# Optimization experiments

Measured on AMD Instinct MI355X. Metric: run time of the kernel, lower is better.

Reference implementation:

```python
import jax, jax.numpy as jnp
import numpy as np

B, S, T = 256, 64, 20
VIN, VOUT, E, H = 32000, 32000, 100, 1024
START_IDX = 1


def gru_cell(gi, h, W_hh, b_hh):
    # gi: precomputed input-side gates [B,3H] (order r,z,n as in PyTorch)
    gh = h @ W_hh.T + b_hh
    ir, iz, inn = jnp.split(gi, 3, axis=-1)
    hr, hz, hn = jnp.split(gh, 3, axis=-1)
    r = jax.nn.sigmoid(ir + hr)
    z = jax.nn.sigmoid(iz + hz)
    n = jnp.tanh(inn + r * hn)
    return (1.0 - z) * n + z * h


def setup_inputs() -> dict:
    key = jax.random.key(0)
    ks = jax.random.split(key, 16)
    sc = 0.05
    inputs = jax.random.randint(ks[0], (B, S), 0, VIN)
    targets = jax.random.randint(ks[1], (B, T), 0, VOUT)
    lengths = jax.random.randint(ks[2], (B,), 1, S + 1)
    h0_enc = jax.random.normal(ks[3], (1, B, H))
    E_enc = jax.random.normal(ks[4], (VIN, E)) * sc
    E_dec = jax.random.normal(ks[5], (VOUT, E)) * sc
    W_ih_e = jax.random.normal(ks[6], (3 * H, E)) * sc
    W_hh_e = jax.random.normal(ks[7], (3 * H, H)) * sc
    b_ih_e = jax.random.normal(ks[8], (3 * H,)) * sc
    b_hh_e = jax.random.normal(ks[9], (3 * H,)) * sc
    W_ih_d = jax.random.normal(ks[10], (3 * H, E + H)) * sc
    W_hh_d = jax.random.normal(ks[11], (3 * H, H)) * sc
    b_ih_d = jax.random.normal(ks[12], (3 * H,)) * sc
    b_hh_d = jax.random.normal(ks[13], (3 * H,)) * sc
    W_fc = jax.random.normal(ks[14], (VOUT, H)) * sc
    b_fc = jax.random.normal(ks[15], (VOUT,)) * sc
    return dict(inputs=inputs, targets=targets, lengths=lengths, h0_enc=h0_enc,
                E_enc=E_enc, E_dec=E_dec,
                W_ih_e=W_ih_e, W_hh_e=W_hh_e, b_ih_e=b_ih_e, b_hh_e=b_hh_e,
                W_ih_d=W_ih_d, W_hh_d=W_hh_d, b_ih_d=b_ih_d, b_hh_d=b_hh_d,
                W_fc=W_fc, b_fc=b_fc)


def reference(inputs, targets, lengths, h0_enc, E_enc, E_dec,
              W_ih_e, W_hh_e, b_ih_e, b_hh_e,
              W_ih_d, W_hh_d, b_ih_d, b_hh_d, W_fc, b_fc):
    Bsz, Slen = inputs.shape
    Tlen = targets.shape[1]
    # ---- Encoder GRU over padded inputs ----
    emb = E_enc[inputs]                       # [B,S,E]
    gi_all = emb @ W_ih_e.T + b_ih_e          # [B,S,3H] input-side gates, precomputed

    def enc_step(h, gi):
        h2 = gru_cell(gi, h, W_hh_e, b_hh_e)
        return h2, h2

    _, hs = jax.lax.scan(enc_step, h0_enc[0], jnp.swapaxes(gi_all, 0, 1))  # hs: [S,B,H]
    # pack_padded_sequence semantics: final hidden = hidden at step lengths-1
    context = hs[lengths - 1, jnp.arange(Bsz)]  # [B,H]

    # ---- Decoder: teacher-forced tokens are [start, targets[:,1:T-1]] ----
    dec_tokens = jnp.concatenate(
        [jnp.full((Bsz, 1), START_IDX, dtype=targets.dtype), targets[:, 1:Tlen - 1]], axis=1)  # [B,T-1]
    demb = E_dec[dec_tokens]                  # [B,T-1,E]
    ctx_b = jnp.broadcast_to(context[:, None, :], (Bsz, Tlen - 1, context.shape[-1]))
    x = jnp.concatenate([demb, ctx_b], axis=-1)          # [B,T-1,E+H]
    gi_d = x @ W_ih_d.T + b_ih_d                          # [B,T-1,3H]
    real = targets[:, 1:].T                               # [T-1,B]

    def dec_step(carry, inp):
        h, loss = carry
        gi, y = inp
        h2 = gru_cell(gi, h, W_hh_d, b_hh_d)
        logits = h2 @ W_fc.T + b_fc                       # [B,V]
        logp = jax.nn.log_softmax(logits, axis=-1)
        ce = -jnp.take_along_axis(logp, y[:, None], axis=1)[:, 0]  # [B]
        mask = (y >= 1).astype(logits.dtype)
        # faithful to: mean(CrossEntropyLoss(reduction='mean') * mask)
        step_loss = jnp.mean(ce) * jnp.mean(mask)
        return (h2, loss + step_loss), None

    init = (context, jnp.asarray(0.0, context.dtype))
    (_, loss), _ = jax.lax.scan(dec_step, init, (jnp.swapaxes(gi_d, 0, 1), real))
    return loss / Tlen
```

## Files before the change

### kernel.cpp

```cpp
#include <hip/hip_runtime.h>
#include <stdint.h>

#define BB 256
#define SS 64
#define TT 20
#define HH 1024
#define EE 100
#define G3 3072
#define G4 4096
#define KE 1152
#define VV 32000

typedef unsigned short ushort_t;
typedef unsigned long long u64_t;
typedef short bf16x8 __attribute__((ext_vector_type(8)));
typedef float f32x4 __attribute__((ext_vector_type(4)));

#define DEV static __device__ __forceinline__

DEV float bf2f(ushort_t h) {
    union { uint32_t u; float f; } c; c.u = ((uint32_t)h) << 16; return c.f;
}
DEV ushort_t f2bf(float x) {
    union { float f; uint32_t u; } c; c.f = x;
    uint32_t r = (c.u + 0x7fffu + ((c.u >> 16) & 1u)) >> 16;
    return (ushort_t)r;
}
DEV float sigm(float x) { return 1.f / (1.f + expf(-x)); }

DEV void storeC(float* p, float v) { *p = v; }
DEV void storeC(ushort_t* p, float v) { *p = f2bf(v); }

DEV u64_t ald(const void* p) {
    return __hip_atomic_load((const u64_t*)p, __ATOMIC_RELAXED, __HIP_MEMORY_SCOPE_AGENT);
}
DEV void ast(void* p, u64_t v) {
    __hip_atomic_store((u64_t*)p, v, __ATOMIC_RELAXED, __HIP_MEMORY_SCOPE_AGENT);
}

#define MFMA16(a, b, c) __builtin_amdgcn_mfma_f32_16x16x32_bf16(a, b, c, 0, 0, 0)

#define LGKM_BARRIER()                                         \
    do {                                                       \
        asm volatile("s_waitcnt lgkmcnt(0)" ::: "memory");     \
        __builtin_amdgcn_s_barrier();                          \
    } while (0)

DEV void groupbar(int* ctr, int target) {
    __syncthreads();
    if (threadIdx.x == 0) {
        __hip_atomic_fetch_add(ctr, 1, __ATOMIC_RELAXED, __HIP_MEMORY_SCOPE_AGENT);
        while (__hip_atomic_load(ctr, __ATOMIC_RELAXED, __HIP_MEMORY_SCOPE_AGENT) < target)
            __builtin_amdgcn_s_sleep(2);
    }
    __syncthreads();
    asm volatile("" ::: "memory");
}

__global__ void prep_w(const float* __restrict__ W_hh_e, const float* __restrict__ W_ih_e,
                       const float* __restrict__ W_ih_d,
                       ushort_t* __restrict__ W_enc_big, ushort_t* __restrict__ W_dec_pad) {
    int idx = blockIdx.x * 256 + threadIdx.x;
    int n = idx / 144, kc = (idx - n * 144) * 8;
    ushort_t o[8];
    if (n < G4) {
        if (kc < HH) {
            if (n < G3) {
#pragma unroll
                for (int u = 0; u < 8; ++u) o[u] = f2bf(W_hh_e[(size_t)n * HH + kc + u]);
            } else {
#pragma unroll
                for (int u = 0; u < 8; ++u) o[u] = 0;
            }
        } else {
            int kk = kc - HH;
#pragma unroll
            for (int u = 0; u < 8; ++u) {
                int k2 = kk + u;
                ushort_t v = 0;
                if (k2 < EE) {
                    if (n < 2048) v = f2bf(W_ih_e[(size_t)n * EE + k2]);
                    else if (n >= G3) v = f2bf(W_ih_e[(size_t)(n - HH) * EE + k2]);
                }
                o[u] = v;
            }
        }
        *(int4*)(W_enc_big + (size_t)n * KE + kc) = *(int4*)o;
    } else {
        int nd = n - G4;
        if (kc < 128) {
#pragma unroll
            for (int u = 0; u < 8; ++u) {
                int k2 = kc + u;
                o[u] = (k2 < EE) ? f2bf(W_ih_d[(size_t)nd * 1124 + k2]) : (ushort_t)0;
            }
        } else {
#pragma unroll
            for (int u = 0; u < 8; ++u) o[u] = f2bf(W_ih_d[(size_t)nd * 1124 + EE + (kc - 128) + u]);
        }
        *(int4*)(W_dec_pad + (size_t)nd * KE + kc) = *(int4*)o;
    }
}

__global__ void conv_w(const float* __restrict__ W_hh_d, const float* __restrict__ W_fc,
                       ushort_t* __restrict__ W_hhd_b, ushort_t* __restrict__ W_fc_b) {
    int idx = blockIdx.x * 256 + threadIdx.x;
    const int N1 = G3 * HH / 8;
    const float* src;
    ushort_t* dst;
    size_t e;
    if (idx < N1) { e = (size_t)idx * 8; src = W_hh_d; dst = W_hhd_b; }
    else { e = (size_t)(idx - N1) * 8; src = W_fc; dst = W_fc_b; }
    float4 a = *(const float4*)(src + e);
    float4 b = *(const float4*)(src + e + 4);
    ushort_t o[8] = {f2bf(a.x), f2bf(a.y), f2bf(a.z), f2bf(a.w),
                     f2bf(b.x), f2bf(b.y), f2bf(b.z), f2bf(b.w)};
    *(int4*)(dst + e) = *(int4*)o;
}

__global__ void prep_x(const int* __restrict__ inputs, const int* __restrict__ targets,
                       const float* __restrict__ h0, const float* __restrict__ E_enc,
                       const float* __restrict__ E_dec,
                       ushort_t* __restrict__ emb_pad, ushort_t* __restrict__ A_enc,
                       ushort_t* __restrict__ A_dec,
                       float* __restrict__ ce_sum, int* __restrict__ bar) {
    int idx = blockIdx.x * 256 + threadIdx.x;
    const int R0 = SS * BB * 128;
    const int R1 = R0 + BB * KE;
    const int R2 = R1 + (TT - 1) * BB * 128;
    const int R3 = R2 + 32 + 1024;
    if (idx < R0) {
        int s = idx >> 15;
        int r = idx & 32767;
        int b = r >> 7, k = r & 127;
        emb_pad[idx] = (k < EE) ? f2bf(E_enc[(size_t)inputs[b * SS + s] * EE + k]) : (ushort_t)0;
    } else if (idx < R1) {
        int i = idx - R0;
        int b = i / KE, c = i - b * KE;
        ushort_t v;
        if (c < HH) v = f2bf(h0[b * HH + c]);
        else { int kk = c - HH; v = (kk < EE) ? f2bf(E_enc[(size_t)inputs[b * SS] * EE + kk]) : (ushort_t)0; }
        A_enc[i] = v;
    } else if (idx < R2) {
        int i = idx - R1;
        int t = i >> 15;
        int r = i & 32767;
        int b = r >> 7, k = r & 127;
        int tok = (t == 0) ? 1 : targets[b * TT + t];
        A_dec[((size_t)(t * BB + b)) * KE + k] = (k < EE) ? f2bf(E_dec[(size_t)tok * EE + k]) : (ushort_t)0;
    } else if (idx < R2 + 32) {
        ce_sum[idx - R2] = 0.f;
    } else if (idx < R3) {
        bar[idx - R2 - 32] = 0;
    }
}

__global__ __launch_bounds__(256) void enc_all(
    ushort_t* __restrict__ A0, ushort_t* __restrict__ A1,
    const ushort_t* __restrict__ W, const float* __restrict__ bi,
    const float* __restrict__ bh, const float* __restrict__ h0,
    const ushort_t* __restrict__ emb_pad, const int* __restrict__ lengths,
    float* __restrict__ ctx_f, ushort_t* __restrict__ ctx_b, int* __restrict__ bar) {
    __shared__ __align__(16) ushort_t As[2][32 * 64];
    __shared__ float gbuf[4][32 * 33];
    int tid = threadIdx.x;
    int bid = blockIdx.x;
    int lane = tid & 63, g = tid >> 6;
    int jb = (bid & 7) * 4 + ((bid >> 3) & 3);
    int mg = bid >> 5;
    int j0 = jb << 5, m0 = mg << 5;
    int* barp = bar + mg * 64;
    int r16 = lane & 15, q = lane >> 4, q8 = q << 3;
    int srow = tid >> 3, skc = (tid & 7) << 3;
    const size_t offA = (size_t)(m0 + srow) * KE + skc;
    const int sx = (srow & 7) << 3;
    const int sw = (srow << 6) + (skc ^ sx);
    const ushort_t* wb0 = W + (size_t)(g * 1024 + j0 + r16) * KE + q8;
    const ushort_t* wb1 = wb0 + (size_t)16 * KE;
    int m = tid & 31, jc0 = (tid >> 5) << 2;
    int bgl = m0 + m, gjj = j0 + jc0;
    int len1 = lengths[bgl] - 1;
    float bir[4], bhr[4], biz[4], bhz[4], bhn[4], bin[4];
#pragma unroll
    for (int u = 0; u < 4; ++u) {
        int jg = gjj + u;
        bir[u] = bi[jg];        bhr[u] = bh[jg];
        biz[u] = bi[1024 + jg]; bhz[u] = bh[1024 + jg];
        bhn[u] = bh[2048 + jg]; bin[u] = bi[2048 + jg];
    }
    float hreg[4];
#pragma unroll
    for (int u = 0; u < 4; ++u) hreg[u] = h0[(size_t)bgl * HH + gjj + u];

#pragma unroll 1
    for (int s = 0; s < SS; ++s) {
        const ushort_t* Ain = (s & 1) ? A1 : A0;
        ushort_t* Aout = (s & 1) ? A0 : A1;
        const ushort_t* ap = Ain + offA;
        f32x4 zero = {0.f, 0.f, 0.f, 0.f};
        f32x4 acc[2][2];
        acc[0][0] = zero; acc[0][1] = zero; acc[1][0] = zero; acc[1][1] = zero;
        u64_t t0a = ald(ap), t0b = ald(ap + 4);
        u64_t b0a = ald(ap + 64), b0b = ald(ap + 68);
        u64_t b1a = ald(ap + 128), b1b = ald(ap + 132);
        bf16x8 wf00 = *(const bf16x8*)(wb0);
        bf16x8 wf01 = *(const bf16x8*)(wb1);
        bf16x8 wf10 = *(const bf16x8*)(wb0 + 32);
        bf16x8 wf11 = *(const bf16x8*)(wb1 + 32);
        { union { u64_t u[2]; int4 v; } st; st.u[0] = t0a; st.u[1] = t0b;
          *(int4*)(As[0] + sw) = st.v; }
        __syncthreads();
        const int NC = KE / 64;
#pragma unroll
        for (int c = 0; c < NC; ++c) {
            int kn = (c + 1) << 6;
            bf16x8 wn00, wn01, wn10, wn11;
            if (c + 1 < NC) {
                union { u64_t u[2]; int4 v; } st;
                if (c & 1) { st.u[0] = b1a; st.u[1] = b1b; }
                else       { st.u[0] = b0a; st.u[1] = b0b; }
                *(int4*)(As[(c + 1) & 1] + sw) = st.v;
                if (c + 3 < NC) {
                    int kf = (c + 3) << 6;
                    if (c & 1) { b1a = ald(ap + kf); b1b = ald(ap + kf + 4); }
                    else       { b0a = ald(ap + kf); b0b = ald(ap + kf + 4); }
                }
                wn00 = *(const bf16x8*)(wb0 + kn);
                wn01 = *(const bf16x8*)(wb1 + kn);
                wn10 = *(const bf16x8*)(wb0 + kn + 32);
                wn11 = *(const bf16x8*)(wb1 + kn + 32);
            }
            const ushort_t* Ab = As[c & 1];
#pragma unroll
            for (int i = 0; i < 2; ++i) {
                int row = (i << 4) + r16;
                int xr = (row & 7) << 3;
                bf16x8 af0 = *(const bf16x8*)(Ab + (row << 6) + (q8 ^ xr));
                bf16x8 af1 = *(const bf16x8*)(Ab + (row << 6) + ((q8 + 32) ^ xr));
                acc[i][0] = MFMA16(af0, wf00, acc[i][0]);
                acc[i][1] = MFMA16(af0, wf01, acc[i][1]);
                acc[i][0] = MFMA16(af1, wf10, acc[i][0]);
                acc[i][1] = MFMA16(af1, wf11, acc[i][1]);
            }
            if (c + 1 < NC) { wf00 = wn00; wf01 = wn01; wf10 = wn10; wf11 = wn11; }
            LGKM_BARRIER();
        }
#pragma unroll
        for (int i = 0; i < 2; ++i)
#pragma unroll
            for (int j2 = 0; j2 < 2; ++j2)
#pragma unroll
                for (int r = 0; r < 4; ++r)
                    gbuf[g][(i * 16 + q * 4 + r) * 33 + j2 * 16 + r16] = acc[i][j2][r];
        __syncthreads();
        int sel = (len1 == s);
        const float* gp0 = &gbuf[0][m * 33 + jc0];
        const float* gp1 = &gbuf[1][m * 33 + jc0];
        const float* gp2 = &gbuf[2][m * 33 + jc0];
        const float* gp3 = &gbuf[3][m * 33 + jc0];
        union { ushort_t s4[4]; u64_t u; } hb;
#pragma unroll
        for (int u = 0; u < 4; ++u) {
            float rr = sigm(gp0[u] + bir[u] + bhr[u]);
            float zz = sigm(gp1[u] + biz[u] + bhz[u]);
            float hn = gp2[u] + bhn[u];
            float inn = gp3[u] + bin[u];
            float nn = tanhf(inn + rr * hn);
            float h2 = (1.f - zz) * nn + zz * hreg[u];
            hreg[u] = h2;
            hb.s4[u] = f2bf(h2);
        }
        ast(Aout + (size_t)bgl * KE + gjj, hb.u);
        if (sel) {
            size_t hi = (size_t)bgl * 1024 + gjj;
            union { float f[2]; u64_t u; } c0, c1;
            c0.f[0] = hreg[0]; c0.f[1] = hreg[1];
            c1.f[0] = hreg[2]; c1.f[1] = hreg[3];
            ast(ctx_f + hi, c0.u); ast(ctx_f + hi + 2, c1.u);
            ast(ctx_b + hi, hb.u);
        }
        if (jb == 0 && s + 1 < SS) {
            int rr2 = tid >> 3, c0e = (tid & 7) << 4;
            const ushort_t* esrc = emb_pad + ((size_t)(s + 1) * BB + m0 + rr2) * 128 + c0e;
            union { int4 v; u64_t u[2]; } e0, e1;
            e0.v = *(const int4*)esrc;
            e1.v = *(const int4*)(esrc + 8);
            ushort_t* dst = Aout + (size_t)(m0 + rr2) * KE + 1024 + c0e;
            ast(dst, e0.u[0]); ast(dst + 4, e0.u[1]);
            ast(dst + 8, e1.u[0]); ast(dst + 12, e1.u[1]);
        }
        if (s + 1 < SS) groupbar(barp, (s + 1) * 32);
    }
}

__global__ void fill_ctx(const ushort_t* __restrict__ ctx_b, ushort_t* __restrict__ A_dec) {
    int idx = blockIdx.x * 256 + threadIdx.x;
    int t = idx >> 18;
    int r = idx & 262143;
    int b = r >> 10;
    int k = r & 1023;
    A_dec[((size_t)(t * BB + b)) * KE + 128 + k] = ctx_b[r];
}

template <typename OutT>
__global__ __launch_bounds__(256) void gemm128(const ushort_t* __restrict__ A,
                                               const ushort_t* __restrict__ W,
                                               OutT* __restrict__ C,
                                               int K, int lda, int ldw, int ldc) {
    __shared__ ushort_t As[2][128 * 32];
    __shared__ ushort_t Bs[2][128 * 32];
    int tid = threadIdx.x;
    int lane = tid & 63, wave = tid >> 6;
    int m0 = blockIdx.y << 7, n0 = blockIdx.x << 7;
    int row0 = tid >> 2, kc0 = (tid & 3) << 3;
    const ushort_t* a0p = A + (size_t)(m0 + row0) * lda + kc0;
    const ushort_t* a1p = A + (size_t)(m0 + row0 + 64) * lda + kc0;
    const ushort_t* w0p = W + (size_t)(n0 + row0) * ldw + kc0;
    const ushort_t* w1p = W + (size_t)(n0 + row0 + 64) * ldw + kc0;
    int mq = (wave >> 1) << 6, nq = (wave & 1) << 6;
    int r16 = lane & 15, q8 = (lane >> 4) << 3;
    const int sx = ((row0 >> 1) & 3) << 3;
    const int sw0 = (row0 << 5) + (kc0 ^ sx);
    const int sw1 = ((row0 + 64) << 5) + (kc0 ^ sx);
    f32x4 zero4 = {0.f, 0.f, 0.f, 0.f};
    f32x4 acc[4][4];
#pragma unroll
    for (int i = 0; i < 4; ++i)
#pragma unroll
        for (int j = 0; j < 4; ++j) acc[i][j] = zero4;
    int4 va0 = *(const int4*)(a0p);
    int4 va1 = *(const int4*)(a1p);
    int4 vb0 = *(const int4*)(w0p);
    int4 vb1 = *(const int4*)(w1p);
    *(int4*)(As[0] + sw0) = va0;
    *(int4*)(As[0] + sw1) = va1;
    *(int4*)(Bs[0] + sw0) = vb0;
    *(int4*)(Bs[0] + sw1) = vb1;
    va0 = *(const int4*)(a0p + 32);
    va1 = *(const int4*)(a1p + 32);
    vb0 = *(const int4*)(w0p + 32);
    vb1 = *(const int4*)(w1p + 32);
    __syncthreads();
    int p = 0;
    for (int k0 = 0; k0 < K; k0 += 32) {
        int kn = k0 + 32;
        if (kn < K) {
            *(int4*)(As[p ^ 1] + sw0) = va0;
            *(int4*)(As[p ^ 1] + sw1) = va1;
            *(int4*)(Bs[p ^ 1] + sw0) = vb0;
            *(int4*)(Bs[p ^ 1] + sw1) = vb1;
            if (kn + 32 < K) {
                va0 = *(const int4*)(a0p + kn + 32);
                va1 = *(const int4*)(a1p + kn + 32);
                vb0 = *(const int4*)(w0p + kn + 32);
                vb1 = *(const int4*)(w1p + kn + 32);
            }
        }
        bf16x8 af[4], bfv[4];
#pragma unroll
        for (int i = 0; i < 4; ++i) {
            int ar = mq + i * 16 + r16;
            af[i] = *(const bf16x8*)(As[p] + (ar << 5) + (q8 ^ ((((ar) >> 1) & 3) << 3)));
        }
#pragma unroll
        for (int j = 0; j < 4; ++j) {
            int br = nq + j * 16 + r16;
            bfv[j] = *(const bf16x8*)(Bs[p] + (br << 5) + (q8 ^ ((((br) >> 1) & 3) << 3)));
        }
#pragma unroll
        for (int i = 0; i < 4; ++i)
#pragma unroll
            for (int j = 0; j < 4; ++j) acc[i][j] = MFMA16(af[i], bfv[j], acc[i][j]);
        LGKM_BARRIER();
        p ^= 1;
    }
    int rbase = (lane >> 4) << 2;
#pragma unroll
    for (int i = 0; i < 4; ++i)
#pragma unroll
        for (int j = 0; j < 4; ++j)
#pragma unroll
            for (int r = 0; r < 4; ++r)
                storeC(&C[(size_t)(m0 + mq + i * 16 + rbase + r) * ldc + (n0 + nq + j * 16 + r16)],
                       acc[i][j][r]);
}

__global__ __launch_bounds__(256) void dec_all(
    const ushort_t* __restrict__ ctx_b, ushort_t* __restrict__ H_all,
    const ushort_t* __restrict__ W, const ushort_t* __restrict__ gi_all,
    const float* __restrict__ bi, const float* __restrict__ bh,
    const float* __restrict__ ctx_f, int* __restrict__ bar) {
    __shared__ __align__(16) ushort_t As[2][32 * 64];
    __shared__ float gbuf[3][32 * 33];
    int tid = threadIdx.x;
    int bid = blockIdx.x;
    int lane = tid & 63, g = tid >> 6;
    int jb = (bid & 7) * 4 + ((bid >> 3) & 3);
    int mg = bid >> 5;
    int j0 = jb << 5, m0 = mg << 5;
    int* barp = bar + 512 + mg * 64;
    int r16 = lane & 15, q = lane >> 4, q8 = q << 3;
    int srow = tid >> 3, skc = (tid & 7) << 3;
    const size_t offA = (size_t)(m0 + srow) * HH + skc;
    const int sx = (srow & 7) << 3;
    const int sw = (srow << 6) + (skc ^ sx);
    const ushort_t* wb0 = W + (size_t)(g * 1024 + j0 + r16) * HH + q8;
    const ushort_t* wb1 = wb0 + (size_t)16 * HH;
    int m = tid & 31, jc0 = (tid >> 5) << 2;
    int bgl = m0 + m, gjj = j0 + jc0;
    float bir[4], bhr[4], biz[4], bhz[4], bhn[4], bin[4];
#pragma unroll
    for (int u = 0; u < 4; ++u) {
        int jg = gjj + u;
        bir[u] = bi[jg];        bhr[u] = bh[jg];
        biz[u] = bi[1024 + jg]; bhz[u] = bh[1024 + jg];
        bhn[u] = bh[2048 + jg]; bin[u] = bi[2048 + jg];
    }
    float hreg[4];
#pragma unroll
    for (int u = 0; u < 4; ++u) hreg[u] = ctx_f[(size_t)bgl * HH + gjj + u];

#pragma unroll 1
    for (int t = 0; t < TT - 1; ++t) {
        const ushort_t* Ain = t ? (H_all + (size_t)(t - 1) * BB * HH) : ctx_b;
        ushort_t* Aout = H_all + (size_t)t * BB * HH;
        const ushort_t* ap = Ain + offA;
        f32x4 zero = {0.f, 0.f, 0.f, 0.f};
        f32x4 acc[2][2];
        acc[0][0] = zero; acc[0][1] = zero; acc[1][0] = zero; acc[1][1] = zero;
        u64_t t0a = ald(ap), t0b = ald(ap + 4);
        u64_t b0a = ald(ap + 64), b0b = ald(ap + 68);
        u64_t b1a = ald(ap + 128), b1b = ald(ap + 132);
        bf16x8 wf00 = {0, 0, 0, 0, 0, 0, 0, 0}, wf01 = wf00, wf10 = wf00, wf11 = wf00;
        if (g < 3) {
            wf00 = *(const bf16x8*)(wb0);
            wf01 = *(const bf16x8*)(wb1);
            wf10 = *(const bf16x8*)(wb0 + 32);
            wf11 = *(const bf16x8*)(wb1 + 32);
        }
        { union { u64_t u[2]; int4 v; } st; st.u[0] = t0a; st.u[1] = t0b;
          *(int4*)(As[0] + sw) = st.v; }
        __syncthreads();
        const int NC = HH / 64;
#pragma unroll
        for (int c = 0; c < NC; ++c) {
            int kn = (c + 1) << 6;
            bf16x8 wn00, wn01, wn10, wn11;
            if (c + 1 < NC) {
                union { u64_t u[2]; int4 v; } st;
                if (c & 1) { st.u[0] = b1a; st.u[1] = b1b; }
                else       { st.u[0] = b0a; st.u[1] = b0b; }
                *(int4*)(As[(c + 1) & 1] + sw) = st.v;
                if (c + 3 < NC) {
                    int kf = (c + 3) << 6;
                    if (c & 1) { b1a = ald(ap + kf); b1b = ald(ap + kf + 4); }
                    else       { b0a = ald(ap + kf); b0b = ald(ap + kf + 4); }
                }
                if (g < 3) {
                    wn00 = *(const bf16x8*)(wb0 + kn);
                    wn01 = *(const bf16x8*)(wb1 + kn);
                    wn10 = *(const bf16x8*)(wb0 + kn + 32);
                    wn11 = *(const bf16x8*)(wb1 + kn + 32);
                }
            }
            if (g < 3) {
                const ushort_t* Ab = As[c & 1];
#pragma unroll
                for (int i = 0; i < 2; ++i) {
                    int row = (i << 4) + r16;
                    int xr = (row & 7) << 3;
                    bf16x8 af0 = *(const bf16x8*)(Ab + (row << 6) + (q8 ^ xr));
                    bf16x8 af1 = *(const bf16x8*)(Ab + (row << 6) + ((q8 + 32) ^ xr));
                    acc[i][0] = MFMA16(af0, wf00, acc[i][0]);
                    acc[i][1] = MFMA16(af0, wf01, acc[i][1]);
                    acc[i][0] = MFMA16(af1, wf10, acc[i][0]);
                    acc[i][1] = MFMA16(af1, wf11, acc[i][1]);
                }
                if (c + 1 < NC) { wf00 = wn00; wf01 = wn01; wf10 = wn10; wf11 = wn11; }
            }
            LGKM_BARRIER();
        }
        if (g < 3) {
#pragma unroll
            for (int i = 0; i < 2; ++i)
#pragma unroll
                for (int j2 = 0; j2 < 2; ++j2)
#pragma unroll
                    for (int r = 0; r < 4; ++r)
                        gbuf[g][(i * 16 + q * 4 + r) * 33 + j2 * 16 + r16] = acc[i][j2][r];
        }
        __syncthreads();
        const ushort_t* gib = gi_all + ((size_t)t * BB + bgl) * G3;
        union { u64_t u; ushort_t s4[4]; } gr, gz, gn;
        gr.u = *(const u64_t*)(gib + gjj);
        gz.u = *(const u64_t*)(gib + 1024 + gjj);
        gn.u = *(const u64_t*)(gib + 2048 + gjj);
        const float* gp0 = &gbuf[0][m * 33 + jc0];
        const float* gp1 = &gbuf[1][m * 33 + jc0];
        const float* gp2 = &gbuf[2][m * 33 + jc0];
        union { ushort_t s4[4]; u64_t u; } hb;
#pragma unroll
        for (int u = 0; u < 4; ++u) {
            float rr = sigm(gp0[u] + bhr[u] + bf2f(gr.s4[u]) + bir[u]);
            float zz = sigm(gp1[u] + bhz[u] + bf2f(gz.s4[u]) + biz[u]);
            float hn = gp2[u] + bhn[u];
            float inn = bf2f(gn.s4[u]) + bin[u];
            float nn = tanhf(inn + rr * hn);
            float h2 = (1.f - zz) * nn + zz * hreg[u];
            hreg[u] = h2;
            hb.s4[u] = f2bf(h2);
        }
        ast(Aout + (size_t)bgl * 1024 + gjj, hb.u);
        if (t + 1 < TT - 1) groupbar(barp, (t + 1) * 32);
    }
}

__global__ __launch_bounds__(256) void logits_ce(
    const ushort_t* __restrict__ A, const ushort_t* __restrict__ Wf,
    const float* __restrict__ bfc, const int* __restrict__ targets,
    float* __restrict__ part_max, float* __restrict__ part_sum,
    float* __restrict__ xt) {
    int bid = blockIdx.x;
    int xcd = bid & 7;
    int slot = bid >> 3;
    int n_t = slot / 5;
    int m_t = xcd * 5 + (slot - n_t * 5);
    if (m_t >= (TT - 1) * BB / 128) return;
    __shared__ ushort_t As[2][128 * 32];
    __shared__ ushort_t Bs[2][128 * 32];
    __shared__ float wm[128][2], ws2[128][2];
    int tid = threadIdx.x;
    int lane = tid & 63, wave = tid >> 6;
    int m0 = m_t << 7, n0 = n_t << 7;
    int row0 = tid >> 2, kc0 = (tid & 3) << 3;
    const ushort_t* a0p = A + (size_t)(m0 + row0) * HH + kc0;
    const ushort_t* a1p = A + (size_t)(m0 + row0 + 64) * HH + kc0;
    const ushort_t* w0p = Wf + (size_t)(n0 + row0) * HH + kc0;
    const ushort_t* w1p = Wf + (size_t)(n0 + row0 + 64) * HH + kc0;
    int mq = (wave >> 1) << 6, nq = (wave & 1) << 6;
    int r16 = lane & 15, q = lane >> 4, q8 = q << 3;
    const int sx = ((row0 >> 1) & 3) << 3;
    const int sw0 = (row0 << 5) + (kc0 ^ sx);
    const int sw1 = ((row0 + 64) << 5) + (kc0 ^ sx);
    f32x4 zero4 = {0.f, 0.f, 0.f, 0.f};
    f32x4 acc[4][4];
#pragma unroll
    for (int i = 0; i < 4; ++i)
#pragma unroll
        for (int j = 0; j < 4; ++j) acc[i][j] = zero4;
    int4 va0 = *(const int4*)(a0p);
    int4 va1 = *(const int4*)(a1p);
    int4 vb0 = *(const int4*)(w0p);
    int4 vb1 = *(const int4*)(w1p);
    *(int4*)(As[0] + sw0) = va0;
    *(int4*)(As[0] + sw1) = va1;
    *(int4*)(Bs[0] + sw0) = vb0;
    *(int4*)(Bs[0] + sw1) = vb1;
    va0 = *(const int4*)(a0p + 32);
    va1 = *(const int4*)(a1p + 32);
    vb0 = *(const int4*)(w0p + 32);
    vb1 = *(const int4*)(w1p + 32);
    __syncthreads();
    int p = 0;
    for (int k0 = 0; k0 < HH; k0 += 32) {
        int kn = k0 + 32;
        if (kn < HH) {
            *(int4*)(As[p ^ 1] + sw0) = va0;
            *(int4*)(As[p ^ 1] + sw1) = va1;
            *(int4*)(Bs[p ^ 1] + sw0) = vb0;
            *(int4*)(Bs[p ^ 1] + sw1) = vb1;
            if (kn + 32 < HH) {
                va0 = *(const int4*)(a0p + kn + 32);
                va1 = *(const int4*)(a1p + kn + 32);
                vb0 = *(const int4*)(w0p + kn + 32);
                vb1 = *(const int4*)(w1p + kn + 32);
            }
        }
        bf16x8 af[4], bfv[4];
#pragma unroll
        for (int i = 0; i < 4; ++i) {
            int ar = mq + i * 16 + r16;
            af[i] = *(const bf16x8*)(As[p] + (ar << 5) + (q8 ^ ((((ar) >> 1) & 3) << 3)));
        }
#pragma unroll
        for (int j = 0; j < 4; ++j) {
            int br = nq + j * 16 + r16;
            bfv[j] = *(const bf16x8*)(Bs[p] + (br << 5) + (q8 ^ ((((br) >> 1) & 3) << 3)));
        }
#pragma unroll
        for (int i = 0; i < 4; ++i)
#pragma unroll
            for (int j = 0; j < 4; ++j) acc[i][j] = MFMA16(af[i], bfv[j], acc[i][j]);
        LGKM_BARRIER();
        p ^= 1;
    }
    float bias[4];
#pragma unroll
    for (int j2 = 0; j2 < 4; ++j2) bias[j2] = bfc[n0 + nq + j2 * 16 + r16];
    int nw = wave & 1;
#pragma unroll
    for (int i = 0; i < 4; ++i) {
#pragma unroll
        for (int r = 0; r < 4; ++r) {
            int rloc = mq + i * 16 + q * 4 + r;
            int brow = m0 + rloc;
            int y = targets[(brow & 255) * TT + (brow >> 8) + 1];
            float v[4];
            float mx = -3.0e38f;
#pragma unroll
            for (int j2 = 0; j2 < 4; ++j2) {
                v[j2] = acc[i][j2][r] + bias[j2];
                if (n0 + nq + j2 * 16 + r16 == y) xt[brow] = v[j2];
                mx = fmaxf(mx, v[j2]);
            }
#pragma unroll
            for (int d = 1; d < 16; d <<= 1) mx = fmaxf(mx, __shfl_xor(mx, d, 64));
            float se = 0.f;
#pragma unroll
            for (int j2 = 0; j2 < 4; ++j2) se += expf(v[j2] - mx);
#pragma unroll
            for (int d = 1; d < 16; d <<= 1) se += __shfl_xor(se, d, 64);
            if (r16 == 0) { wm[rloc][nw] = mx; ws2[rloc][nw] = se; }
        }
    }
    __syncthreads();
    if (tid < 128) {
        float m0v = wm[tid][0], m1v = wm[tid][1];
        float M = fmaxf(m0v, m1v);
        float S = ws2[tid][0] * expf(m0v - M) + ws2[tid][1] * expf(m1v - M);
        int brow = m0 + tid;
        part_max[(size_t)brow * 256 + n_t] = M;
        part_sum[(size_t)brow * 256 + n_t] = S;
    }
}

__global__ void ce_merge(const float* __restrict__ pm, const float* __restrict__ ps,
                         const float* __restrict__ xt, float* __restrict__ ce_sum) {
    int row = blockIdx.x * 4 + (threadIdx.x >> 6);
    int lane = threadIdx.x & 63;
    const float* pmr = pm + (size_t)row * 256;
    const float* psr = ps + (size_t)row * 256;
    float lm[4];
    int cnt = 0;
    float mx = -3.0e38f;
    for (int i = lane; i < 250; i += 64) { float v = pmr[i]; lm[cnt++] = v; mx = fmaxf(mx, v); }
    for (int d = 1; d < 64; d <<= 1) mx = fmaxf(mx, __shfl_xor(mx, d, 64));
    float s = 0.f;
    cnt = 0;
    for (int i = lane; i < 250; i += 64) { s += psr[i] * expf(lm[cnt++] - mx); }
    for (int d = 1; d < 64; d <<= 1) s += __shfl_xor(s, d, 64);
    if (lane == 0) atomicAdd(&ce_sum[row >> 8], mx + logf(s) - xt[row]);
}

__global__ void finalize(const float* __restrict__ ce_sum, const int* __restrict__ targets,
                         float* __restrict__ out) {
    int lane = threadIdx.x;
    float term = 0.f;
    if (lane < TT - 1) {
        int msum = 0;
        for (int b = 0; b < BB; ++b) msum += (targets[b * TT + lane + 1] >= 1) ? 1 : 0;
        term = (ce_sum[lane] * (1.f / BB)) * ((float)msum * (1.f / BB));
    }
    for (int off = 32; off > 0; off >>= 1) term += __shfl_down(term, off, 64);
    if (lane == 0) out[0] = term * (1.f / TT);
}

extern "C" void kernel_launch(void* const* d_in, const int* in_sizes, int n_in,
                              void* d_out, int out_size, void* d_ws, size_t ws_size,
                              hipStream_t stream) {
    const int* inputs = (const int*)d_in[0];
    const int* targets = (const int*)d_in[1];
    const int* lengths = (const int*)d_in[2];
    const float* h0 = (const float*)d_in[3];
    const float* E_enc = (const float*)d_in[4];
    const float* E_dec = (const float*)d_in[5];
    const float* W_ih_e = (const float*)d_in[6];
    const float* W_hh_e = (const float*)d_in[7];
    const float* b_ih_e = (const float*)d_in[8];
    const float* b_hh_e = (const float*)d_in[9];
    const float* W_ih_d = (const float*)d_in[10];
    const float* W_hh_d = (const float*)d_in[11];
    const float* b_ih_d = (const float*)d_in[12];
    const float* b_hh_d = (const float*)d_in[13];
    const float* W_fc = (const float*)d_in[14];
    const float* b_fc = (const float*)d_in[15];

    char* ws = (char*)d_ws;
    size_t off = 0;
    auto alloc = [&](size_t bytes) -> char* {
        char* p = ws + off;
        off += (bytes + 255) & ~(size_t)255;
        return p;
    };
    const int MROWS = (TT - 1) * BB;
    ushort_t* W_enc_big = (ushort_t*)alloc((size_t)G4 * KE * 2);
    ushort_t* W_dec_pad = (ushort_t*)alloc((size_t)G3 * KE * 2);
    ushort_t* W_hhd_b = (ushort_t*)alloc((size_t)G3 * HH * 2);
    ushort_t* W_fc_b = (ushort_t*)alloc((size_t)VV * HH * 2);
    ushort_t* emb_pad = (ushort_t*)alloc((size_t)SS * BB * 128 * 2);
    ushort_t* A_enc0 = (ushort_t*)alloc((size_t)BB * KE * 2);
    ushort_t* A_enc1 = (ushort_t*)alloc((size_t)BB * KE * 2);
    ushort_t* A_dec = (ushort_t*)alloc((size_t)MROWS * KE * 2);
    ushort_t* gi_dec = (ushort_t*)alloc((size_t)MROWS * G3 * 2);
    ushort_t* H_all = (ushort_t*)alloc((size_t)MROWS * HH * 2);
    float* ctx_f = (float*)alloc((size_t)BB * HH * 4);
    ushort_t* ctx_b = (ushort_t*)alloc((size_t)BB * HH * 2);
    float* part_max = (float*)alloc((size_t)MROWS * 256 * 4);
    float* part_sum = (float*)alloc((size_t)MROWS * 256 * 4);
    float* xt = (float*)alloc((size_t)MROWS * 4);
    float* ce_sum = (float*)alloc(64 * 4);
    int* bar = (int*)alloc(1024 * 4);

    prep_w<<<(G4 + G3) * (KE / 8) / 256, 256, 0, stream>>>(W_hh_e, W_ih_e, W_ih_d,
                                                           W_enc_big, W_dec_pad);
    conv_w<<<(G3 * HH + VV * HH) / 8 / 256, 256, 0, stream>>>(W_hh_d, W_fc, W_hhd_b, W_fc_b);
    {
        int nx = SS * BB * 128 + BB * KE + (TT - 1) * BB * 128 + 32 + 1024;
        prep_x<<<(nx + 255) / 256, 256, 0, stream>>>(inputs, targets, h0, E_enc, E_dec,
                                                     emb_pad, A_enc0, A_dec, ce_sum, bar);
    }

    enc_all<<<256, 256, 0, stream>>>(A_enc0, A_enc1, W_enc_big, b_ih_e, b_hh_e,
                                     h0, emb_pad, lengths, ctx_f, ctx_b, bar);

    fill_ctx<<<((TT - 1) * BB * HH) / 256, 256, 0, stream>>>(ctx_b, A_dec);
    gemm128<ushort_t><<<dim3(G3 / 128, MROWS / 128), 256, 0, stream>>>(
        A_dec, W_dec_pad, gi_dec, KE, KE, KE, G3);

    dec_all<<<256, 256, 0, stream>>>(ctx_b, H_all, W_hhd_b, gi_dec,
                                     b_ih_d, b_hh_d, ctx_f, bar);

    logits_ce<<<10000, 256, 0, stream>>>(H_all, W_fc_b, b_fc, targets,
                                         part_max, part_sum, xt);
    ce_merge<<<MROWS / 4, 256, 0, stream>>>(part_max, part_sum, xt, ce_sum);

    finalize<<<1, 64, 0, stream>>>(ce_sum, targets, (float*)d_out);
}
```

Baseline: 1.800 ms.

## Halve batch tile in persistent GRU kernels, launch 512 blocks, preload A rows

The persistent encoder and decoder recurrence kernels now give each block 16 batch rows instead of 32, so the grid doubles to 512 blocks at two blocks per CU. Each block loads all of its hidden-state chunks into registers at the start of a step instead of running a rolling three-stage prefetch. The barrier area is enlarged to hold the extra group counters. The intent is to spread the serial recurrence across more CUs and cut per-step latency. In exchange, every block re-reads the full weight slice, so weight traffic per step doubles, and the grid-wide spin barriers now have twice as many participants.

```diff
diff --git a/kernel.cpp b/kernel.cpp
--- a/kernel.cpp
+++ b/kernel.cpp
@@ -36,6 +36,9 @@
 }
 DEV void ast(void* p, u64_t v) {
     __hip_atomic_store((u64_t*)p, v, __ATOMIC_RELAXED, __HIP_MEMORY_SCOPE_AGENT);
+}
+DEV void ast32(void* p, uint32_t v) {
+    __hip_atomic_store((uint32_t*)p, v, __ATOMIC_RELAXED, __HIP_MEMORY_SCOPE_AGENT);
 }
 
 #define MFMA16(a, b, c) __builtin_amdgcn_mfma_f32_16x16x32_bf16(a, b, c, 0, 0, 0)
@@ -128,7 +131,7 @@
     const int R0 = SS * BB * 128;
     const int R1 = R0 + BB * KE;
     const int R2 = R1 + (TT - 1) * BB * 128;
-    const int R3 = R2 + 32 + 1024;
+    const int R3 = R2 + 32 + 2048;
     if (idx < R0) {
         int s = idx >> 15;
         int r = idx & 32767;
@@ -155,112 +158,95 @@
     }
 }
 
-__global__ __launch_bounds__(256) void enc_all(
+__global__ __launch_bounds__(256, 2) void enc_all(
     ushort_t* __restrict__ A0, ushort_t* __restrict__ A1,
     const ushort_t* __restrict__ W, const float* __restrict__ bi,
     const float* __restrict__ bh, const float* __restrict__ h0,
     const ushort_t* __restrict__ emb_pad, const int* __restrict__ lengths,
     float* __restrict__ ctx_f, ushort_t* __restrict__ ctx_b, int* __restrict__ bar) {
-    __shared__ __align__(16) ushort_t As[2][32 * 64];
-    __shared__ float gbuf[4][32 * 33];
+    __shared__ __align__(16) ushort_t As[2][16 * 64];
+    __shared__ float gbuf[4][16 * 33];
     int tid = threadIdx.x;
     int bid = blockIdx.x;
     int lane = tid & 63, g = tid >> 6;
     int jb = (bid & 7) * 4 + ((bid >> 3) & 3);
     int mg = bid >> 5;
-    int j0 = jb << 5, m0 = mg << 5;
+    int j0 = jb << 5, m0 = mg << 4;
     int* barp = bar + mg * 64;
     int r16 = lane & 15, q = lane >> 4, q8 = q << 3;
-    int srow = tid >> 3, skc = (tid & 7) << 3;
+    int srow = tid >> 4, skc = (tid & 15) << 2;
     const size_t offA = (size_t)(m0 + srow) * KE + skc;
-    const int sx = (srow & 7) << 3;
-    const int sw = (srow << 6) + (skc ^ sx);
+    const int sw = (srow << 6) + (skc ^ ((srow & 7) << 3));
     const ushort_t* wb0 = W + (size_t)(g * 1024 + j0 + r16) * KE + q8;
     const ushort_t* wb1 = wb0 + (size_t)16 * KE;
-    int m = tid & 31, jc0 = (tid >> 5) << 2;
+    int m = tid & 15, jc0 = (tid >> 4) << 1;
     int bgl = m0 + m, gjj = j0 + jc0;
     int len1 = lengths[bgl] - 1;
-    float bir[4], bhr[4], biz[4], bhz[4], bhn[4], bin[4];
-#pragma unroll
-    for (int u = 0; u < 4; ++u) {
+    float bir[2], bhr[2], biz[2], bhz[2], bhn[2], bin[2];
+#pragma unroll
+    for (int u = 0; u < 2; ++u) {
         int jg = gjj + u;
         bir[u] = bi[jg];        bhr[u] = bh[jg];
         biz[u] = bi[1024 + jg]; bhz[u] = bh[1024 + jg];
         bhn[u] = bh[2048 + jg]; bin[u] = bi[2048 + jg];
     }
-    float hreg[4];
-#pragma unroll
-    for (int u = 0; u < 4; ++u) hreg[u] = h0[(size_t)bgl * HH + gjj + u];
-
+    float hreg[2];
+#pragma unroll
+    for (int u = 0; u < 2; ++u) hreg[u] = h0[(size_t)bgl * HH + gjj + u];
+
+    const int NC = KE / 64;
 #pragma unroll 1
     for (int s = 0; s < SS; ++s) {
         const ushort_t* Ain = (s & 1) ? A1 : A0;
         ushort_t* Aout = (s & 1) ? A0 : A1;
         const ushort_t* ap = Ain + offA;
+        u64_t areg[NC];
+#pragma unroll
+        for (int c = 0; c < NC; ++c) areg[c] = ald(ap + (c << 6));
         f32x4 zero = {0.f, 0.f, 0.f, 0.f};
-        f32x4 acc[2][2];
-        acc[0][0] = zero; acc[0][1] = zero; acc[1][0] = zero; acc[1][1] = zero;
-        u64_t t0a = ald(ap), t0b = ald(ap + 4);
-        u64_t b0a = ald(ap + 64), b0b = ald(ap + 68);
-        u64_t b1a = ald(ap + 128), b1b = ald(ap + 132);
+        f32x4 acc0 = zero, acc1 = zero;
         bf16x8 wf00 = *(const bf16x8*)(wb0);
         bf16x8 wf01 = *(const bf16x8*)(wb1);
         bf16x8 wf10 = *(const bf16x8*)(wb0 + 32);
         bf16x8 wf11 = *(const bf16x8*)(wb1 + 32);
-        { union { u64_t u[2]; int4 v; } st; st.u[0] = t0a; st.u[1] = t0b;
-          *(int4*)(As[0] + sw) = st.v; }
-        __syncthreads();
-        const int NC = KE / 64;
+        *(u64_t*)(As[0] + sw) = areg[0];
+        LGKM_BARRIER();
 #pragma unroll
         for (int c = 0; c < NC; ++c) {
-            int kn = (c + 1) << 6;
             bf16x8 wn00, wn01, wn10, wn11;
             if (c + 1 < NC) {
-                union { u64_t u[2]; int4 v; } st;
-                if (c & 1) { st.u[0] = b1a; st.u[1] = b1b; }
-                else       { st.u[0] = b0a; st.u[1] = b0b; }
-                *(int4*)(As[(c + 1) & 1] + sw) = st.v;
-                if (c + 3 < NC) {
-                    int kf = (c + 3) << 6;
-                    if (c & 1) { b1a = ald(ap + kf); b1b = ald(ap + kf + 4); }
-                    else       { b0a = ald(ap + kf); b0b = ald(ap + kf + 4); }
-                }
+                *(u64_t*)(As[(c + 1) & 1] + sw) = areg[c + 1];
+                int kn = (c + 1) << 6;
                 wn00 = *(const bf16x8*)(wb0 + kn);
                 wn01 = *(const bf16x8*)(wb1 + kn);
                 wn10 = *(const bf16x8*)(wb0 + kn + 32);
                 wn11 = *(const bf16x8*)(wb1 + kn + 32);
             }
             const ushort_t* Ab = As[c & 1];
-#pragma unroll
-            for (int i = 0; i < 2; ++i) {
-                int row = (i << 4) + r16;
-                int xr = (row & 7) << 3;
-                bf16x8 af0 = *(const bf16x8*)(Ab + (row << 6) + (q8 ^ xr));
-                bf16x8 af1 = *(const bf16x8*)(Ab + (row << 6) + ((q8 + 32) ^ xr));
-                acc[i][0] = MFMA16(af0, wf00, acc[i][0]);
-                acc[i][1] = MFMA16(af0, wf01, acc[i][1]);
-                acc[i][0] = MFMA16(af1, wf10, acc[i][0]);
-                acc[i][1] = MFMA16(af1, wf11, acc[i][1]);
-            }
+            int xr = (r16 & 7) << 3;
+            bf16x8 af0 = *(const bf16x8*)(Ab + (r16 << 6) + (q8 ^ xr));
+            bf16x8 af1 = *(const bf16x8*)(Ab + (r16 << 6) + ((q8 + 32) ^ xr));
+            acc0 = MFMA16(af0, wf00, acc0);
+            acc1 = MFMA16(af0, wf01, acc1);
+            acc0 = MFMA16(af1, wf10, acc0);
+            acc1 = MFMA16(af1, wf11, acc1);
             if (c + 1 < NC) { wf00 = wn00; wf01 = wn01; wf10 = wn10; wf11 = wn11; }
             LGKM_BARRIER();
         }
 #pragma unroll
-        for (int i = 0; i < 2; ++i)
-#pragma unroll
-            for (int j2 = 0; j2 < 2; ++j2)
-#pragma unroll
-                for (int r = 0; r < 4; ++r)
-                    gbuf[g][(i * 16 + q * 4 + r) * 33 + j2 * 16 + r16] = acc[i][j2][r];
+        for (int r = 0; r < 4; ++r) {
+            gbuf[g][(q * 4 + r) * 33 + r16] = acc0[r];
+            gbuf[g][(q * 4 + r) * 33 + 16 + r16] = acc1[r];
+        }
         __syncthreads();
         int sel = (len1 == s);
         const float* gp0 = &gbuf[0][m * 33 + jc0];
         const float* gp1 = &gbuf[1][m * 33 + jc0];
         const float* gp2 = &gbuf[2][m * 33 + jc0];
         const float* gp3 = &gbuf[3][m * 33 + jc0];
-        union { ushort_t s4[4]; u64_t u; } hb;
-#pragma unroll
-        for (int u = 0; u < 4; ++u) {
+        union { ushort_t s2[2]; uint32_t u; } hb;
+#pragma unroll
+        for (int u = 0; u < 2; ++u) {
             float rr = sigm(gp0[u] + bir[u] + bhr[u]);
             float zz = sigm(gp1[u] + biz[u] + bhz[u]);
             float hn = gp2[u] + bhn[u];
@@ -268,26 +254,23 @@
             float nn = tanhf(inn + rr * hn);
             float h2 = (1.f - zz) * nn + zz * hreg[u];
             hreg[u] = h2;
-            hb.s4[u] = f2bf(h2);
-        }
-        ast(Aout + (size_t)bgl * KE + gjj, hb.u);
+            hb.s2[u] = f2bf(h2);
+        }
+        ast32(Aout + (size_t)bgl * KE + gjj, hb.u);
         if (sel) {
             size_t hi = (size_t)bgl * 1024 + gjj;
-            union { float f[2]; u64_t u; } c0, c1;
-            c0.f[0] = hreg[0]; c0.f[1] = hreg[1];
-            c1.f[0] = hreg[2]; c1.f[1] = hreg[3];
-            ast(ctx_f + hi, c0.u); ast(ctx_f + hi + 2, c1.u);
-            ast(ctx_b + hi, hb.u);
+            union { float f[2]; u64_t u; } cf;
+            cf.f[0] = hreg[0]; cf.f[1] = hreg[1];
+            ast(ctx_f + hi, cf.u);
+            ast32(ctx_b + hi, hb.u);
         }
         if (jb == 0 && s + 1 < SS) {
-            int rr2 = tid >> 3, c0e = (tid & 7) << 4;
+            int rr2 = tid >> 4, c0e = (tid & 15) << 3;
             const ushort_t* esrc = emb_pad + ((size_t)(s + 1) * BB + m0 + rr2) * 128 + c0e;
-            union { int4 v; u64_t u[2]; } e0, e1;
+            union { int4 v; u64_t u[2]; } e0;
             e0.v = *(const int4*)esrc;
-            e1.v = *(const int4*)(esrc + 8);
             ushort_t* dst = Aout + (size_t)(m0 + rr2) * KE + 1024 + c0e;
             ast(dst, e0.u[0]); ast(dst + 4, e0.u[1]);
-            ast(dst + 8, e1.u[0]); ast(dst + 12, e1.u[1]);
         }
         if (s + 1 < SS) groupbar(barp, (s + 1) * 32);
     }
@@ -385,52 +368,51 @@
                        acc[i][j][r]);
 }
 
-__global__ __launch_bounds__(256) void dec_all(
+__global__ __launch_bounds__(256, 2) void dec_all(
     const ushort_t* __restrict__ ctx_b, ushort_t* __restrict__ H_all,
     const ushort_t* __restrict__ W, const ushort_t* __restrict__ gi_all,
     const float* __restrict__ bi, const float* __restrict__ bh,
     const float* __restrict__ ctx_f, int* __restrict__ bar) {
-    __shared__ __align__(16) ushort_t As[2][32 * 64];
-    __shared__ float gbuf[3][32 * 33];
+    __shared__ __align__(16) ushort_t As[2][16 * 64];
+    __shared__ float gbuf[3][16 * 33];
     int tid = threadIdx.x;
     int bid = blockIdx.x;
     int lane = tid & 63, g = tid >> 6;
     int jb = (bid & 7) * 4 + ((bid >> 3) & 3);
     int mg = bid >> 5;
-    int j0 = jb << 5, m0 = mg << 5;
-    int* barp = bar + 512 + mg * 64;
+    int j0 = jb << 5, m0 = mg << 4;
+    int* barp = bar + 1024 + mg * 64;
     int r16 = lane & 15, q = lane >> 4, q8 = q << 3;
-    int srow = tid >> 3, skc = (tid & 7) << 3;
+    int srow = tid >> 4, skc = (tid & 15) << 2;
     const size_t offA = (size_t)(m0 + srow) * HH + skc;
-    const int sx = (srow & 7) << 3;
-    const int sw = (srow << 6) + (skc ^ sx);
+    const int sw = (srow << 6) + (skc ^ ((srow & 7) << 3));
     const ushort_t* wb0 = W + (size_t)(g * 1024 + j0 + r16) * HH + q8;
     const ushort_t* wb1 = wb0 + (size_t)16 * HH;
-    int m = tid & 31, jc0 = (tid >> 5) << 2;
+    int m = tid & 15, jc0 = (tid >> 4) << 1;
     int bgl = m0 + m, gjj = j0 + jc0;
-    float bir[4], bhr[4], biz[4], bhz[4], bhn[4], bin[4];
-#pragma unroll
-    for (int u = 0; u < 4; ++u) {
+    float bir[2], bhr[2], biz[2], bhz[2], bhn[2], bin[2];
+#pragma unroll
+    for (int u = 0; u < 2; ++u) {
         int jg = gjj + u;
         bir[u] = bi[jg];        bhr[u] = bh[jg];
         biz[u] = bi[1024 + jg]; bhz[u] = bh[1024 + jg];
         bhn[u] = bh[2048 + jg]; bin[u] = bi[2048 + jg];
     }
-    float hreg[4];
-#pragma unroll
-    for (int u = 0; u < 4; ++u) hreg[u] = ctx_f[(size_t)bgl * HH + gjj + u];
-
+    float hreg[2];
+#pragma unroll
+    for (int u = 0; u < 2; ++u) hreg[u] = ctx_f[(size_t)bgl * HH + gjj + u];
+
+    const int NC = HH / 64;
 #pragma unroll 1
     for (int t = 0; t < TT - 1; ++t) {
         const ushort_t* Ain = t ? (H_all + (size_t)(t - 1) * BB * HH) : ctx_b;
         ushort_t* Aout = H_all + (size_t)t * BB * HH;
         const ushort_t* ap = Ain + offA;
+        u64_t areg[NC];
+#pragma unroll
+        for (int c = 0; c < NC; ++c) areg[c] = ald(ap + (c << 6));
         f32x4 zero = {0.f, 0.f, 0.f, 0.f};
-        f32x4 acc[2][2];
-        acc[0][0] = zero; acc[0][1] = zero; acc[1][0] = zero; acc[1][1] = zero;
-        u64_t t0a = ald(ap), t0b = ald(ap + 4);
-        u64_t b0a = ald(ap + 64), b0b = ald(ap + 68);
-        u64_t b1a = ald(ap + 128), b1b = ald(ap + 132);
+        f32x4 acc0 = zero, acc1 = zero;
         bf16x8 wf00 = {0, 0, 0, 0, 0, 0, 0, 0}, wf01 = wf00, wf10 = wf00, wf11 = wf00;
         if (g < 3) {
             wf00 = *(const bf16x8*)(wb0);
@@ -438,25 +420,15 @@
             wf10 = *(const bf16x8*)(wb0 + 32);
             wf11 = *(const bf16x8*)(wb1 + 32);
         }
-        { union { u64_t u[2]; int4 v; } st; st.u[0] = t0a; st.u[1] = t0b;
-          *(int4*)(As[0] + sw) = st.v; }
-        __syncthreads();
-        const int NC = HH / 64;
+        *(u64_t*)(As[0] + sw) = areg[0];
+        LGKM_BARRIER();
 #pragma unroll
         for (int c = 0; c < NC; ++c) {
-            int kn = (c + 1) << 6;
             bf16x8 wn00, wn01, wn10, wn11;
             if (c + 1 < NC) {
-                union { u64_t u[2]; int4 v; } st;
-                if (c & 1) { st.u[0] = b1a; st.u[1] = b1b; }
-                else       { st.u[0] = b0a; st.u[1] = b0b; }
-                *(int4*)(As[(c + 1) & 1] + sw) = st.v;
-                if (c + 3 < NC) {
-                    int kf = (c + 3) << 6;
-                    if (c & 1) { b1a = ald(ap + kf); b1b = ald(ap + kf + 4); }
-                    else       { b0a = ald(ap + kf); b0b = ald(ap + kf + 4); }
-                }
+                *(u64_t*)(As[(c + 1) & 1] + sw) = areg[c + 1];
                 if (g < 3) {
+                    int kn = (c + 1) << 6;
                     wn00 = *(const bf16x8*)(wb0 + kn);
                     wn01 = *(const bf16x8*)(wb1 + kn);
                     wn10 = *(const bf16x8*)(wb0 + kn + 32);
@@ -465,52 +437,46 @@
             }
             if (g < 3) {
                 const ushort_t* Ab = As[c & 1];
-#pragma unroll
-                for (int i = 0; i < 2; ++i) {
-                    int row = (i << 4) + r16;
-                    int xr = (row & 7) << 3;
-                    bf16x8 af0 = *(const bf16x8*)(Ab + (row << 6) + (q8 ^ xr));
-                    bf16x8 af1 = *(const bf16x8*)(Ab + (row << 6) + ((q8 + 32) ^ xr));
-                    acc[i][0] = MFMA16(af0, wf00, acc[i][0]);
-                    acc[i][1] = MFMA16(af0, wf01, acc[i][1]);
-                    acc[i][0] = MFMA16(af1, wf10, acc[i][0]);
-                    acc[i][1] = MFMA16(af1, wf11, acc[i][1]);
-                }
+                int xr = (r16 & 7) << 3;
+                bf16x8 af0 = *(const bf16x8*)(Ab + (r16 << 6) + (q8 ^ xr));
+                bf16x8 af1 = *(const bf16x8*)(Ab + (r16 << 6) + ((q8 + 32) ^ xr));
+                acc0 = MFMA16(af0, wf00, acc0);
+                acc1 = MFMA16(af0, wf01, acc1);
+                acc0 = MFMA16(af1, wf10, acc0);
+                acc1 = MFMA16(af1, wf11, acc1);
                 if (c + 1 < NC) { wf00 = wn00; wf01 = wn01; wf10 = wn10; wf11 = wn11; }
             }
             LGKM_BARRIER();
         }
         if (g < 3) {
 #pragma unroll
-            for (int i = 0; i < 2; ++i)
-#pragma unroll
-                for (int j2 = 0; j2 < 2; ++j2)
-#pragma unroll
-                    for (int r = 0; r < 4; ++r)
-                        gbuf[g][(i * 16 + q * 4 + r) * 33 + j2 * 16 + r16] = acc[i][j2][r];
+            for (int r = 0; r < 4; ++r) {
+                gbuf[g][(q * 4 + r) * 33 + r16] = acc0[r];
+                gbuf[g][(q * 4 + r) * 33 + 16 + r16] = acc1[r];
+            }
         }
         __syncthreads();
         const ushort_t* gib = gi_all + ((size_t)t * BB + bgl) * G3;
-        union { u64_t u; ushort_t s4[4]; } gr, gz, gn;
-        gr.u = *(const u64_t*)(gib + gjj);
-        gz.u = *(const u64_t*)(gib + 1024 + gjj);
-        gn.u = *(const u64_t*)(gib + 2048 + gjj);
+        union { uint32_t u; ushort_t s2[2]; } gr, gz, gn;
+        gr.u = *(const uint32_t*)(gib + gjj);
+        gz.u = *(const uint32_t*)(gib + 1024 + gjj);
+        gn.u = *(const uint32_t*)(gib + 2048 + gjj);
         const float* gp0 = &gbuf[0][m * 33 + jc0];
         const float* gp1 = &gbuf[1][m * 33 + jc0];
         const float* gp2 = &gbuf[2][m * 33 + jc0];
-        union { ushort_t s4[4]; u64_t u; } hb;
-#pragma unroll
-        for (int u = 0; u < 4; ++u) {
-            float rr = sigm(gp0[u] + bhr[u] + bf2f(gr.s4[u]) + bir[u]);
-            float zz = sigm(gp1[u] + bhz[u] + bf2f(gz.s4[u]) + biz[u]);
+        union { ushort_t s2[2]; uint32_t u; } hb;
+#pragma unroll
+        for (int u = 0; u < 2; ++u) {
+            float rr = sigm(gp0[u] + bhr[u] + bf2f(gr.s2[u]) + bir[u]);
+            float zz = sigm(gp1[u] + bhz[u] + bf2f(gz.s2[u]) + biz[u]);
             float hn = gp2[u] + bhn[u];
-            float inn = bf2f(gn.s4[u]) + bin[u];
+            float inn = bf2f(gn.s2[u]) + bin[u];
             float nn = tanhf(inn + rr * hn);
             float h2 = (1.f - zz) * nn + zz * hreg[u];
             hreg[u] = h2;
-            hb.s4[u] = f2bf(h2);
-        }
-        ast(Aout + (size_t)bgl * 1024 + gjj, hb.u);
+            hb.s2[u] = f2bf(h2);
+        }
+        ast32(Aout + (size_t)bgl * 1024 + gjj, hb.u);
         if (t + 1 < TT - 1) groupbar(barp, (t + 1) * 32);
     }
 }
@@ -709,25 +675,25 @@
     float* part_sum = (float*)alloc((size_t)MROWS * 256 * 4);
     float* xt = (float*)alloc((size_t)MROWS * 4);
     float* ce_sum = (float*)alloc(64 * 4);
-    int* bar = (int*)alloc(1024 * 4);
+    int* bar = (int*)alloc(2048 * 4);
 
     prep_w<<<(G4 + G3) * (KE / 8) / 256, 256, 0, stream>>>(W_hh_e, W_ih_e, W_ih_d,
                                                            W_enc_big, W_dec_pad);
     conv_w<<<(G3 * HH + VV * HH) / 8 / 256, 256, 0, stream>>>(W_hh_d, W_fc, W_hhd_b, W_fc_b);
     {
-        int nx = SS * BB * 128 + BB * KE + (TT - 1) * BB * 128 + 32 + 1024;
+        int nx = SS * BB * 128 + BB * KE + (TT - 1) * BB * 128 + 32 + 2048;
         prep_x<<<(nx + 255) / 256, 256, 0, stream>>>(inputs, targets, h0, E_enc, E_dec,
                                                      emb_pad, A_enc0, A_dec, ce_sum, bar);
     }
 
-    enc_all<<<256, 256, 0, stream>>>(A_enc0, A_enc1, W_enc_big, b_ih_e, b_hh_e,
+    enc_all<<<512, 256, 0, stream>>>(A_enc0, A_enc1, W_enc_big, b_ih_e, b_hh_e,
                                      h0, emb_pad, lengths, ctx_f, ctx_b, bar);
 
     fill_ctx<<<((TT - 1) * BB * HH) / 256, 256, 0, stream>>>(ctx_b, A_dec);
     gemm128<ushort_t><<<dim3(G3 / 128, MROWS / 128), 256, 0, stream>>>(
         A_dec, W_dec_pad, gi_dec, KE, KE, KE, G3);
 
-    dec_all<<<256, 256, 0, stream>>>(ctx_b, H_all, W_hhd_b, gi_dec,
+    dec_all<<<512, 256, 0, stream>>>(ctx_b, H_all, W_hhd_b, gi_dec,
                                      b_ih_d, b_hh_d, ctx_f, bar);
 
     logits_ce<<<10000, 256, 0, stream>>>(H_all, W_fc_b, b_fc, targets,
```

Result: slower. 2.363 ms (+31.3%).
